# Performance work log

Measured on AMD Instinct MI355X. Metric: run time of the kernel, lower is better.

The kernel has to match this reference:

```python
import math
import jax, jax.numpy as jnp
import numpy as np

B, S, D, H = 2, 2048, 1024, 16
DK = D // H


def setup_inputs() -> dict:
    key = jax.random.key(0)
    ks = jax.random.split(key, 12)
    scale = 1.0 / math.sqrt(D)
    inp = {
        "q": jax.random.normal(ks[0], (B, S, D), jnp.float32),
        "k": jax.random.normal(ks[1], (B, S, D), jnp.float32),
        "v": jax.random.normal(ks[2], (B, S, D), jnp.float32),
        # causal mask, broadcast over batch and heads (mask==0 -> -inf)
        "mask": jnp.tril(jnp.ones((S, S), jnp.int32))[None, None, :, :],
        "Wq": jax.random.normal(ks[3], (D, D), jnp.float32) * scale,
        "bq": jnp.zeros((D,), jnp.float32),
        "Wk": jax.random.normal(ks[4], (D, D), jnp.float32) * scale,
        "bk": jnp.zeros((D,), jnp.float32),
        "Wv": jax.random.normal(ks[5], (D, D), jnp.float32) * scale,
        "bv": jnp.zeros((D,), jnp.float32),
        "Wo": jax.random.normal(ks[6], (D, D), jnp.float32) * scale,
        "bo": jnp.zeros((D,), jnp.float32),
    }
    return inp


def reference(q, k, v, mask, Wq, bq, Wk, bk, Wv, bv, Wo, bo):
    def proj(x, W, b):
        # [B,S,D] -> [B,H,S,DK]
        return (x @ W + b).reshape(B, -1, H, DK).transpose(0, 2, 1, 3)

    Q = proj(q, Wq, bq)
    K = proj(k, Wk, bk)
    V = proj(v, Wv, bv)
    scores = jnp.einsum("bhqd,bhkd->bhqk", Q, K) / math.sqrt(DK)  # [B,H,S,S]
    scores = jnp.where(mask == 0, -jnp.inf, scores)
    attn = jax.nn.softmax(scores, axis=-1)  # dropout p=0.0 -> identity
    ctx = jnp.einsum("bhqk,bhkd->bhqd", attn, V)
    ctx = ctx.transpose(0, 2, 1, 3).reshape(B, -1, D)  # [B,S,D]
    return ctx @ Wo + bo
```

## Files before the change

### kernel.cpp

```cpp
#include <hip/hip_runtime.h>
#include <stdint.h>

#define BB 2
#define SS 2048
#define DD 1024
#define HH 16
#define DK 64

#define QSCALE 0.1803368801111204f
#define NEGS -1.0e30f

typedef short s16x8 __attribute__((ext_vector_type(8)));
typedef float f32x4 __attribute__((ext_vector_type(4)));
typedef unsigned short u16x4 __attribute__((ext_vector_type(4)));
typedef unsigned int u32x4 __attribute__((ext_vector_type(4)));

static __device__ __forceinline__ unsigned short f2bf(float f) {
  unsigned int u = __builtin_bit_cast(unsigned int, f);
  u = (u + 0x7fffu + ((u >> 16) & 1u)) >> 16;
  return (unsigned short)u;
}

static __device__ __forceinline__ float bf2f(unsigned short s) {
  unsigned int u = ((unsigned int)s) << 16;
  return __builtin_bit_cast(float, u);
}

static __device__ __forceinline__ unsigned int cvtpk(float lo, float hi) {
  unsigned int r;
  asm("v_cvt_pk_bf16_f32 %0, %1, %2" : "=v"(r) : "v"(lo), "v"(hi));
  return r;
}

static __device__ __forceinline__ f32x4 mfma16(s16x8 a, s16x8 b, f32x4 c) {
  return __builtin_amdgcn_mfma_f32_16x16x32_bf16(a, b, c, 0, 0, 0);
}

static __device__ __forceinline__ void gload_lds16(const void* g, void* l) {
  __builtin_amdgcn_global_load_lds(
      (const __attribute__((address_space(1))) unsigned int*)g,
      (__attribute__((address_space(3))) unsigned int*)l, 16, 0, 0);
}

__global__ __launch_bounds__(256) void cvt3_kernel(const float* __restrict__ q,
                                                   const float* __restrict__ k,
                                                   const float* __restrict__ v,
                                                   unsigned short* __restrict__ qb,
                                                   unsigned short* __restrict__ kb,
                                                   unsigned short* __restrict__ vb) {
  int sel = blockIdx.y;
  const float* in = (sel == 0) ? q : ((sel == 1) ? k : v);
  unsigned short* out = (sel == 0) ? qb : ((sel == 1) ? kb : vb);
  int i = blockIdx.x * 256 + threadIdx.x;
  f32x4 vv = ((const f32x4*)in)[i];
  u16x4 o;
  o.x = f2bf(vv.x); o.y = f2bf(vv.y); o.z = f2bf(vv.z); o.w = f2bf(vv.w);
  ((u16x4*)out)[i] = o;
}

__global__ __launch_bounds__(256) void transpose_w4_kernel(const float* __restrict__ Wq,
                                                           const float* __restrict__ Wk,
                                                           const float* __restrict__ Wv,
                                                           const float* __restrict__ Wo,
                                                           unsigned short* __restrict__ WTbase) {
  __shared__ float t[32][33];
  int z = blockIdx.z;
  const float* W = (z == 0) ? Wq : ((z == 1) ? Wk : ((z == 2) ? Wv : Wo));
  float scale = (z == 0) ? QSCALE : 1.0f;
  unsigned short* WT = WTbase + (size_t)z * DD * DD;
  int n0 = blockIdx.x * 32, k0 = blockIdx.y * 32;
  int tx = threadIdx.x, ty = threadIdx.y;
  for (int i = 0; i < 4; ++i)
    t[ty + 8 * i][tx] = W[(size_t)(k0 + ty + 8 * i) * DD + n0 + tx];
  __syncthreads();
  for (int i = 0; i < 4; ++i)
    WT[(size_t)(n0 + ty + 8 * i) * DD + k0 + tx] = f2bf(t[tx][ty + 8 * i] * scale);
}

__global__ __launch_bounds__(256) void gemm_qkv_kernel(
    const unsigned short* __restrict__ qb, const unsigned short* __restrict__ kb,
    const unsigned short* __restrict__ vb, const unsigned short* __restrict__ WTbase,
    const float* __restrict__ bq, const float* __restrict__ bk,
    const float* __restrict__ bv, unsigned short* __restrict__ Qh,
    unsigned short* __restrict__ Kh, unsigned short* __restrict__ VhT) {
  const int K = DD;
  __shared__ __align__(16) unsigned short Alds[128 * 32];
  __shared__ __align__(16) unsigned short Blds[128 * 32];
  int tid = threadIdx.x;
  int lane = tid & 63, wave = tid >> 6;
  int g = lane >> 4, r16 = lane & 15;

  int bid = blockIdx.x;
  int logical = (bid & 7) * 96 + (bid >> 3);
  int y = logical >> 3, xn = logical & 7;
  int seg = y >> 5;
  int m0 = (y & 31) * 128, n0 = xn * 128;
  int wm = (wave >> 1) * 64, wn = (wave & 1) * 64;

  const unsigned short* A = (seg == 0) ? qb : ((seg == 1) ? kb : vb);
  const unsigned short* BT = WTbase + (size_t)seg * DD * DD;
  const float* bias = (seg == 0) ? bq : ((seg == 1) ? bk : bv);
  float bsc = (seg == 0) ? QSCALE : 1.0f;

  f32x4 acc[4][4] = {};

  int c0 = tid, c1 = tid + 256;
  int arow0 = c0 >> 2, arow1 = c1 >> 2;
  int as0 = (c0 & 3) ^ ((arow0 >> 1) & 3);
  int as1 = (c1 & 3) ^ ((arow1 >> 1) & 3);

  for (int k0 = 0; k0 < K; k0 += 32) {
    __syncthreads();
    gload_lds16((const char*)(A + (size_t)(m0 + arow0) * K + k0) + as0 * 16,
                (char*)Alds + wave * 1024);
    gload_lds16((const char*)(A + (size_t)(m0 + arow1) * K + k0) + as1 * 16,
                (char*)Alds + wave * 1024 + 4096);
    gload_lds16((const char*)(BT + (size_t)(n0 + arow0) * K + k0) + as0 * 16,
                (char*)Blds + wave * 1024);
    gload_lds16((const char*)(BT + (size_t)(n0 + arow1) * K + k0) + as1 * 16,
                (char*)Blds + wave * 1024 + 4096);
    __syncthreads();

    s16x8 af[4], bfr[4];
#pragma unroll
    for (int mt = 0; mt < 4; ++mt) {
      int row = wm + mt * 16 + r16;
      int ch = g ^ ((row >> 1) & 3);
      af[mt] = *(const s16x8*)((const char*)Alds + row * 64 + ch * 16);
    }
#pragma unroll
    for (int nt = 0; nt < 4; ++nt) {
      int row = wn + nt * 16 + r16;
      int ch = g ^ ((row >> 1) & 3);
      bfr[nt] = *(const s16x8*)((const char*)Blds + row * 64 + ch * 16);
    }
#pragma unroll
    for (int mt = 0; mt < 4; ++mt)
#pragma unroll
      for (int nt = 0; nt < 4; ++nt)
        acc[mt][nt] = mfma16(af[mt], bfr[nt], acc[mt][nt]);
  }

  unsigned short* outh = (seg == 0) ? Qh : Kh;
#pragma unroll
  for (int nt = 0; nt < 4; ++nt) {
    int col = n0 + wn + nt * 16 + r16;
    int h = col >> 6, dk = col & (DK - 1);
    float bvv = bias[col] * bsc;
#pragma unroll
    for (int mt = 0; mt < 4; ++mt) {
      int row0g = m0 + wm + mt * 16 + g * 4;
      int bb = row0g >> 11, s0 = row0g & (SS - 1);
      if (seg == 2) {
        u16x4 o;
#pragma unroll
        for (int rr = 0; rr < 4; ++rr) o[rr] = f2bf(acc[mt][nt][rr] + bvv);
        *(u16x4*)&VhT[((size_t)(bb * HH + h) * DK + dk) * SS + s0] = o;
      } else {
#pragma unroll
        for (int rr = 0; rr < 4; ++rr) {
          outh[(((size_t)bb * HH + h) * SS + s0 + rr) * DK + dk] =
              f2bf(acc[mt][nt][rr] + bvv);
        }
      }
    }
  }
}

__global__ __launch_bounds__(256) void gemm_out_kernel(const unsigned short* __restrict__ A,
                                                       const unsigned short* __restrict__ BT,
                                                       const float* __restrict__ bias,
                                                       float* __restrict__ out) {
  const int K = DD;
  __shared__ __align__(16) unsigned short Alds[128 * 32];
  __shared__ __align__(16) unsigned short Blds[64 * 32];
  int tid = threadIdx.x;
  int lane = tid & 63, wave = tid >> 6;
  int g = lane >> 4, r16 = lane & 15;

  int bid = blockIdx.x;
  int logical = (bid & 7) * 64 + (bid >> 3);
  int m0 = (logical >> 4) * 128, n0 = (logical & 15) * 64;
  int wm = (wave >> 1) * 64, wn = (wave & 1) * 32;

  f32x4 acc[4][2] = {};

  int c0 = tid, c1 = tid + 256;
  int arow0 = c0 >> 2, arow1 = c1 >> 2;
  int as0 = (c0 & 3) ^ ((arow0 >> 1) & 3);
  int as1 = (c1 & 3) ^ ((arow1 >> 1) & 3);

  for (int k0 = 0; k0 < K; k0 += 32) {
    __syncthreads();
    gload_lds16((const char*)(A + (size_t)(m0 + arow0) * K + k0) + as0 * 16,
                (char*)Alds + wave * 1024);
    gload_lds16((const char*)(A + (size_t)(m0 + arow1) * K + k0) + as1 * 16,
                (char*)Alds + wave * 1024 + 4096);
    gload_lds16((const char*)(BT + (size_t)(n0 + arow0) * K + k0) + as0 * 16,
                (char*)Blds + wave * 1024);
    __syncthreads();

    s16x8 af[4], bfr[2];
#pragma unroll
    for (int mt = 0; mt < 4; ++mt) {
      int row = wm + mt * 16 + r16;
      int ch = g ^ ((row >> 1) & 3);
      af[mt] = *(const s16x8*)((const char*)Alds + row * 64 + ch * 16);
    }
#pragma unroll
    for (int nt = 0; nt < 2; ++nt) {
      int row = wn + nt * 16 + r16;
      int ch = g ^ ((row >> 1) & 3);
      bfr[nt] = *(const s16x8*)((const char*)Blds + row * 64 + ch * 16);
    }
#pragma unroll
    for (int mt = 0; mt < 4; ++mt)
#pragma unroll
      for (int nt = 0; nt < 2; ++nt)
        acc[mt][nt] = mfma16(af[mt], bfr[nt], acc[mt][nt]);
  }

#pragma unroll
  for (int nt = 0; nt < 2; ++nt) {
    int col = n0 + wn + nt * 16 + r16;
    float bvv = bias[col];
#pragma unroll
    for (int mt = 0; mt < 4; ++mt) {
#pragma unroll
      for (int rr = 0; rr < 4; ++rr) {
        int rowg = m0 + wm + mt * 16 + g * 4 + rr;
        out[(size_t)rowg * DD + col] = acc[mt][nt][rr] + bvv;
      }
    }
  }
}

__global__ __launch_bounds__(256) void attn_kernel(const unsigned short* __restrict__ Qh,
                                                   const unsigned short* __restrict__ Kh,
                                                   const unsigned short* __restrict__ VhT,
                                                   unsigned short* __restrict__ ctx,
                                                   unsigned short* __restrict__ Opart,
                                                   float2* __restrict__ mlpart) {
  __shared__ __align__(16) unsigned short Klds[2][64 * 64];
  __shared__ __align__(16) unsigned short Vlds[2][64 * 64];

  int tid = threadIdx.x;
  int lane = tid & 63, wave = tid >> 6;
  int g = lane >> 4, r16 = lane & 15;
  int bid = blockIdx.x;
  int x = bid >> 3;
  int pid = x & 7;
  int hf = (x >> 3) & 1;
  int bh = ((x >> 4) << 3) | (bid & 7);

  int tilesA = hf ? 0 : 2 * pid + 2;
  const int NT = 17;
  int q0A = pid * 128, q0B = (15 - pid) * 128;
  int kvoffB = hf ? (15 - 2 * pid) : 0;

  const unsigned short* Qb = Qh + (size_t)bh * SS * DK;
  const char* Kb = (const char*)(Kh + (size_t)bh * SS * DK);
  const char* Vb = (const char*)(VhT + (size_t)bh * DK * SS);

  int a_ = r16 >> 2, b_ = r16 & 3;
  int rbase = 8 * a_ + b_;
  int sk = b_ + 4 * (a_ & 1);

  int c0 = tid, c1 = tid + 256;
  int row0 = c0 >> 3, row1 = c1 >> 3;
  int skst0 = ((row0 & 3) | (((row0 >> 3) & 1) << 2));
  int skst1 = ((row1 & 3) | (((row1 >> 3) & 1) << 2));
  int kc0 = (c0 & 7) ^ skst0, kc1 = (c1 & 7) ^ skst1;
  int vc0 = (c0 & 7) ^ (row0 & 7), vc1 = (c1 & 7) ^ (row1 & 7);

#define KV_OF(t) ((hf ? (kvoffB + (t)) : (((t) < tilesA) ? (t) : ((t) - tilesA))) * 64)
#define STAGE_KV(buf, kv0)                                                   \
  do {                                                                       \
    gload_lds16(Kb + ((size_t)((kv0) + row0) * 128) + kc0 * 16,              \
                (char*)Klds[buf] + wave * 1024);                             \
    gload_lds16(Kb + ((size_t)((kv0) + row1) * 128) + kc1 * 16,              \
                (char*)Klds[buf] + wave * 1024 + 4096);                      \
    gload_lds16(Vb + ((size_t)row0 * SS + (kv0)) * 2 + vc0 * 16,             \
                (char*)Vlds[buf] + wave * 1024);                             \
    gload_lds16(Vb + ((size_t)row1 * SS + (kv0)) * 2 + vc1 * 16,             \
                (char*)Vlds[buf] + wave * 1024 + 4096);                      \
  } while (0)

  int b = bh >> 4, h = bh & (HH - 1);

  int qw0 = (hf ? q0B : q0A) + wave * 32;
  s16x8 aq[2][2];
#pragma unroll
  for (int mt = 0; mt < 2; ++mt)
#pragma unroll
    for (int kc = 0; kc < 2; ++kc)
      aq[mt][kc] = *(const s16x8*)(Qb + (size_t)(qw0 + mt * 16 + r16) * DK + kc * 32 + g * 8);

  STAGE_KV(0, KV_OF(0));

  f32x4 accd[2][4] = {};
  float mrow[2] = {-INFINITY, -INFINITY};
  float lrow[2] = {0.0f, 0.0f};

  for (int t = 0; t < NT; ++t) {
    if (hf == 0 && t == tilesA) {
#pragma unroll
      for (int mt = 0; mt < 2; ++mt) {
        float inv = 1.0f / lrow[mt];
        int srow = qw0 + mt * 16 + r16;
#pragma unroll
        for (int dsub = 0; dsub < 4; ++dsub) {
          int d0 = dsub * 16 + 4 * g;
          u16x4 o;
#pragma unroll
          for (int rr = 0; rr < 4; ++rr) o[rr] = f2bf(accd[mt][dsub][rr] * inv);
          *(u16x4*)&ctx[(((size_t)b * SS + srow) * HH + h) * DK + d0] = o;
        }
      }
      qw0 = q0B + wave * 32;
#pragma unroll
      for (int mt = 0; mt < 2; ++mt)
#pragma unroll
        for (int kc = 0; kc < 2; ++kc)
          aq[mt][kc] = *(const s16x8*)(Qb + (size_t)(qw0 + mt * 16 + r16) * DK + kc * 32 + g * 8);
#pragma unroll
      for (int mt = 0; mt < 2; ++mt) {
#pragma unroll
        for (int dsub = 0; dsub < 4; ++dsub) accd[mt][dsub] = (f32x4){0.f, 0.f, 0.f, 0.f};
        mrow[mt] = -INFINITY;
        lrow[mt] = 0.0f;
      }
    }

    int kv0 = KV_OF(t);

    __syncthreads();
    if (t + 1 < NT) STAGE_KV((t + 1) & 1, KV_OF(t + 1));

    const char* Kc = (const char*)Klds[t & 1];
    const char* Vc = (const char*)Vlds[t & 1];

    f32x4 sf[2][4] = {};
    __builtin_amdgcn_s_setprio(1);
#pragma unroll
    for (int kc = 0; kc < 2; ++kc) {
      s16x8 bk[4];
#pragma unroll
      for (int nt = 0; nt < 4; ++nt) {
        int row = rbase + 4 * (nt & 1) + 32 * (nt >> 1);
        int ch = (kc * 4 + g) ^ sk;
        bk[nt] = *(const s16x8*)(Kc + row * 128 + ch * 16);
      }
#pragma unroll
      for (int nt = 0; nt < 4; ++nt) {
        sf[0][nt] = mfma16(bk[nt], aq[0][kc], sf[0][nt]);
        sf[1][nt] = mfma16(bk[nt], aq[1][kc], sf[1][nt]);
      }
    }
    __builtin_amdgcn_s_setprio(0);

    s16x8 av[2][4];
#pragma unroll
    for (int c = 0; c < 2; ++c)
#pragma unroll
      for (int dsub = 0; dsub < 4; ++dsub) {
        int row = dsub * 16 + r16;
        int ch = (c * 4 + g) ^ (row & 7);
        av[c][dsub] = *(const s16x8*)(Vc + row * 128 + ch * 16);
      }

    bool domask = (kv0 + 63 > qw0);
    unsigned int pk[2][2][4];
#pragma unroll
    for (int mt = 0; mt < 2; ++mt) {
      if (domask) {
        int thr = qw0 + mt * 16 + r16 - kv0 - 8 * g;
#pragma unroll
        for (int nt = 0; nt < 4; ++nt) {
          int koff = 4 * (nt & 1) + 32 * (nt >> 1);
#pragma unroll
          for (int rr = 0; rr < 4; ++rr)
            if (koff + rr > thr) sf[mt][nt][rr] = NEGS;
        }
      }

      float m0v = fmaxf(fmaxf(sf[mt][0][0], sf[mt][0][1]), fmaxf(sf[mt][0][2], sf[mt][0][3]));
      float m1v = fmaxf(fmaxf(sf[mt][1][0], sf[mt][1][1]), fmaxf(sf[mt][1][2], sf[mt][1][3]));
      float m2v = fmaxf(fmaxf(sf[mt][2][0], sf[mt][2][1]), fmaxf(sf[mt][2][2], sf[mt][2][3]));
      float m3v = fmaxf(fmaxf(sf[mt][3][0], sf[mt][3][1]), fmaxf(sf[mt][3][2], sf[mt][3][3]));
      float tmax = fmaxf(fmaxf(m0v, m1v), fmaxf(m2v, m3v));
      tmax = fmaxf(tmax, __shfl_xor(tmax, 16));
      tmax = fmaxf(tmax, __shfl_xor(tmax, 32));

      if (!__all(tmax <= mrow[mt])) {
        float mn = fmaxf(mrow[mt], tmax);
        float fc = __builtin_amdgcn_exp2f(mrow[mt] - mn);
        lrow[mt] *= fc;
        mrow[mt] = mn;
#pragma unroll
        for (int dsub = 0; dsub < 4; ++dsub)
#pragma unroll
          for (int rr = 0; rr < 4; ++rr) accd[mt][dsub][rr] *= fc;
      }

      float pf[4][4];
#pragma unroll
      for (int nt = 0; nt < 4; ++nt)
#pragma unroll
        for (int rr = 0; rr < 4; ++rr)
          pf[nt][rr] = __builtin_amdgcn_exp2f(sf[mt][nt][rr] - mrow[mt]);
      float s0v = (pf[0][0] + pf[0][1]) + (pf[0][2] + pf[0][3]);
      float s1v = (pf[1][0] + pf[1][1]) + (pf[1][2] + pf[1][3]);
      float s2v = (pf[2][0] + pf[2][1]) + (pf[2][2] + pf[2][3]);
      float s3v = (pf[3][0] + pf[3][1]) + (pf[3][2] + pf[3][3]);
      float su = (s0v + s1v) + (s2v + s3v);
      su += __shfl_xor(su, 16);
      su += __shfl_xor(su, 32);
      lrow[mt] += su;

#pragma unroll
      for (int c = 0; c < 2; ++c) {
        pk[mt][c][0] = cvtpk(pf[2 * c][0], pf[2 * c][1]);
        pk[mt][c][1] = cvtpk(pf[2 * c][2], pf[2 * c][3]);
        pk[mt][c][2] = cvtpk(pf[2 * c + 1][0], pf[2 * c + 1][1]);
        pk[mt][c][3] = cvtpk(pf[2 * c + 1][2], pf[2 * c + 1][3]);
      }
    }

    __builtin_amdgcn_s_setprio(1);
#pragma unroll
    for (int c = 0; c < 2; ++c) {
      s16x8 pb0 = __builtin_bit_cast(s16x8, *(u32x4*)pk[0][c]);
      s16x8 pb1 = __builtin_bit_cast(s16x8, *(u32x4*)pk[1][c]);
#pragma unroll
      for (int dsub = 0; dsub < 4; ++dsub) {
        accd[0][dsub] = mfma16(av[c][dsub], pb0, accd[0][dsub]);
        accd[1][dsub] = mfma16(av[c][dsub], pb1, accd[1][dsub]);
      }
    }
    __builtin_amdgcn_s_setprio(0);
  }

#pragma unroll
  for (int mt = 0; mt < 2; ++mt) {
    size_t prow = ((size_t)bh * 8 + pid) * 128 + wave * 32 + mt * 16 + r16;
    float inv = 1.0f / lrow[mt];
    unsigned short* Op = Opart + ((size_t)hf * 32768 + prow) * 64;
#pragma unroll
    for (int dsub = 0; dsub < 4; ++dsub) {
      int d0 = dsub * 16 + 4 * g;
      u16x4 o;
#pragma unroll
      for (int rr = 0; rr < 4; ++rr) o[rr] = f2bf(accd[mt][dsub][rr] * inv);
      *(u16x4*)&Op[d0] = o;
    }
    if (g == 0) mlpart[(size_t)hf * 32768 + prow] = make_float2(mrow[mt], lrow[mt]);
  }
#undef STAGE_KV
#undef KV_OF
}

__global__ __launch_bounds__(256) void combine_kernel(const unsigned short* __restrict__ Opart,
                                                      const float2* __restrict__ mlpart,
                                                      unsigned short* __restrict__ ctx) {
  int idx = blockIdx.x * 256 + threadIdx.x;
  int row = idx >> 4;
  int d0 = (idx & 15) * 4;
  float2 ml0 = mlpart[row];
  float2 ml1 = mlpart[32768 + row];
  float m = fmaxf(ml0.x, ml1.x);
  float w0 = __builtin_amdgcn_exp2f(ml0.x - m) * ml0.y;
  float w1 = __builtin_amdgcn_exp2f(ml1.x - m) * ml1.y;
  float inv = 1.0f / (w0 + w1);
  w0 *= inv;
  w1 *= inv;
  u16x4 a = *(const u16x4*)(Opart + (size_t)row * 64 + d0);
  u16x4 bb4 = *(const u16x4*)(Opart + ((size_t)32768 + row) * 64 + d0);
  u16x4 o;
#pragma unroll
  for (int j = 0; j < 4; ++j) o[j] = f2bf(bf2f(a[j]) * w0 + bf2f(bb4[j]) * w1);
  int p = row >> 7, rin = row & 127;
  int bh = p >> 3, pid = p & 7;
  int srow = (15 - pid) * 128 + rin;
  int b = bh >> 4, h = bh & (HH - 1);
  *(u16x4*)&ctx[(((size_t)b * SS + srow) * HH + h) * DK + d0] = o;
}

extern "C" void kernel_launch(void* const* d_in, const int* in_sizes, int n_in,
                              void* d_out, int out_size, void* d_ws, size_t ws_size,
                              hipStream_t stream) {
  const float* q = (const float*)d_in[0];
  const float* k = (const float*)d_in[1];
  const float* v = (const float*)d_in[2];
  const float* Wq = (const float*)d_in[4];
  const float* bq = (const float*)d_in[5];
  const float* Wk = (const float*)d_in[6];
  const float* bk = (const float*)d_in[7];
  const float* Wv = (const float*)d_in[8];
  const float* bv = (const float*)d_in[9];
  const float* Wo = (const float*)d_in[10];
  const float* bo = (const float*)d_in[11];

  char* ws = (char*)d_ws;
  const size_t MB = 1ull << 20;
  unsigned short* qb = (unsigned short*)(ws + 0 * MB);
  unsigned short* kb = (unsigned short*)(ws + 8 * MB);
  unsigned short* vb = (unsigned short*)(ws + 16 * MB);
  unsigned short* WTbase = (unsigned short*)(ws + 24 * MB);
  unsigned short* WoT = (unsigned short*)(ws + 30 * MB);
  unsigned short* Qh = (unsigned short*)(ws + 32 * MB);
  unsigned short* Kh = (unsigned short*)(ws + 40 * MB);
  unsigned short* VhT = (unsigned short*)(ws + 48 * MB);
  unsigned short* ctx = (unsigned short*)(ws + 0 * MB);
  unsigned short* Opart = (unsigned short*)(ws + 8 * MB);
  float2* mlpart = (float2*)(ws + 24 * MB);

  const int n4 = BB * SS * DD / 4;

  cvt3_kernel<<<dim3(n4 / 256, 3), 256, 0, stream>>>(q, k, v, qb, kb, vb);

  dim3 tb(32, 8);
  transpose_w4_kernel<<<dim3(32, 32, 4), tb, 0, stream>>>(Wq, Wk, Wv, Wo, WTbase);

  gemm_qkv_kernel<<<768, 256, 0, stream>>>(qb, kb, vb, WTbase,
                                           bq, bk, bv, Qh, Kh, VhT);

  attn_kernel<<<512, 256, 0, stream>>>(Qh, Kh, VhT, ctx, Opart, mlpart);

  combine_kernel<<<2048, 256, 0, stream>>>(Opart, mlpart, ctx);

  gemm_out_kernel<<<512, 256, 0, stream>>>(ctx, WoT, bo, (float*)d_out);
}
```

Baseline: 133.6 us.

## Double-buffer LDS tiles in projection GEMMs and raise priority around MFMAs

Both the QKV projection GEMM and the output projection GEMM now keep two LDS buffers. The next k-tile's global-to-LDS loads are issued before computing on the current tile, and the loop needs one barrier per iteration instead of two. The MFMA block is wrapped in s_setprio so compute waves get scheduling priority. This hides global load latency behind matrix math, at the cost of doubling LDS per block, which may lower occupancy.

```diff
diff --git a/kernel.cpp b/kernel.cpp
--- a/kernel.cpp
+++ b/kernel.cpp
@@ -84,8 +84,8 @@
     const float* __restrict__ bv, unsigned short* __restrict__ Qh,
     unsigned short* __restrict__ Kh, unsigned short* __restrict__ VhT) {
   const int K = DD;
-  __shared__ __align__(16) unsigned short Alds[128 * 32];
-  __shared__ __align__(16) unsigned short Blds[128 * 32];
+  __shared__ __align__(16) unsigned short Alds[2][128 * 32];
+  __shared__ __align__(16) unsigned short Blds[2][128 * 32];
   int tid = threadIdx.x;
   int lane = tid & 63, wave = tid >> 6;
   int g = lane >> 4, r16 = lane & 15;
@@ -109,37 +109,48 @@
   int as0 = (c0 & 3) ^ ((arow0 >> 1) & 3);
   int as1 = (c1 & 3) ^ ((arow1 >> 1) & 3);
 
+#define STAGE_AB(buf, k0)                                                        \
+  do {                                                                           \
+    gload_lds16((const char*)(A + (size_t)(m0 + arow0) * K + (k0)) + as0 * 16,   \
+                (char*)Alds[buf] + wave * 1024);                                 \
+    gload_lds16((const char*)(A + (size_t)(m0 + arow1) * K + (k0)) + as1 * 16,   \
+                (char*)Alds[buf] + wave * 1024 + 4096);                          \
+    gload_lds16((const char*)(BT + (size_t)(n0 + arow0) * K + (k0)) + as0 * 16,  \
+                (char*)Blds[buf] + wave * 1024);                                 \
+    gload_lds16((const char*)(BT + (size_t)(n0 + arow1) * K + (k0)) + as1 * 16,  \
+                (char*)Blds[buf] + wave * 1024 + 4096);                          \
+  } while (0)
+
+  STAGE_AB(0, 0);
+  int cur = 0;
+
   for (int k0 = 0; k0 < K; k0 += 32) {
     __syncthreads();
-    gload_lds16((const char*)(A + (size_t)(m0 + arow0) * K + k0) + as0 * 16,
-                (char*)Alds + wave * 1024);
-    gload_lds16((const char*)(A + (size_t)(m0 + arow1) * K + k0) + as1 * 16,
-                (char*)Alds + wave * 1024 + 4096);
-    gload_lds16((const char*)(BT + (size_t)(n0 + arow0) * K + k0) + as0 * 16,
-                (char*)Blds + wave * 1024);
-    gload_lds16((const char*)(BT + (size_t)(n0 + arow1) * K + k0) + as1 * 16,
-                (char*)Blds + wave * 1024 + 4096);
-    __syncthreads();
+    if (k0 + 32 < K) STAGE_AB(cur ^ 1, k0 + 32);
 
     s16x8 af[4], bfr[4];
 #pragma unroll
     for (int mt = 0; mt < 4; ++mt) {
       int row = wm + mt * 16 + r16;
       int ch = g ^ ((row >> 1) & 3);
-      af[mt] = *(const s16x8*)((const char*)Alds + row * 64 + ch * 16);
+      af[mt] = *(const s16x8*)((const char*)Alds[cur] + row * 64 + ch * 16);
     }
 #pragma unroll
     for (int nt = 0; nt < 4; ++nt) {
       int row = wn + nt * 16 + r16;
       int ch = g ^ ((row >> 1) & 3);
-      bfr[nt] = *(const s16x8*)((const char*)Blds + row * 64 + ch * 16);
-    }
+      bfr[nt] = *(const s16x8*)((const char*)Blds[cur] + row * 64 + ch * 16);
+    }
+    __builtin_amdgcn_s_setprio(1);
 #pragma unroll
     for (int mt = 0; mt < 4; ++mt)
 #pragma unroll
       for (int nt = 0; nt < 4; ++nt)
         acc[mt][nt] = mfma16(af[mt], bfr[nt], acc[mt][nt]);
+    __builtin_amdgcn_s_setprio(0);
+    cur ^= 1;
   }
+#undef STAGE_AB
 
   unsigned short* outh = (seg == 0) ? Qh : Kh;
 #pragma unroll
@@ -172,8 +183,8 @@
                                                        const float* __restrict__ bias,
                                                        float* __restrict__ out) {
   const int K = DD;
-  __shared__ __align__(16) unsigned short Alds[128 * 32];
-  __shared__ __align__(16) unsigned short Blds[64 * 32];
+  __shared__ __align__(16) unsigned short Alds[2][128 * 32];
+  __shared__ __align__(16) unsigned short Blds[2][64 * 32];
   int tid = threadIdx.x;
   int lane = tid & 63, wave = tid >> 6;
   int g = lane >> 4, r16 = lane & 15;
@@ -190,35 +201,46 @@
   int as0 = (c0 & 3) ^ ((arow0 >> 1) & 3);
   int as1 = (c1 & 3) ^ ((arow1 >> 1) & 3);
 
+#define STAGE_AB(buf, k0)                                                        \
+  do {                                                                           \
+    gload_lds16((const char*)(A + (size_t)(m0 + arow0) * K + (k0)) + as0 * 16,   \
+                (char*)Alds[buf] + wave * 1024);                                 \
+    gload_lds16((const char*)(A + (size_t)(m0 + arow1) * K + (k0)) + as1 * 16,   \
+                (char*)Alds[buf] + wave * 1024 + 4096);                          \
+    gload_lds16((const char*)(BT + (size_t)(n0 + arow0) * K + (k0)) + as0 * 16,  \
+                (char*)Blds[buf] + wave * 1024);                                 \
+  } while (0)
+
+  STAGE_AB(0, 0);
+  int cur = 0;
+
   for (int k0 = 0; k0 < K; k0 += 32) {
     __syncthreads();
-    gload_lds16((const char*)(A + (size_t)(m0 + arow0) * K + k0) + as0 * 16,
-                (char*)Alds + wave * 1024);
-    gload_lds16((const char*)(A + (size_t)(m0 + arow1) * K + k0) + as1 * 16,
-                (char*)Alds + wave * 1024 + 4096);
-    gload_lds16((const char*)(BT + (size_t)(n0 + arow0) * K + k0) + as0 * 16,
-                (char*)Blds + wave * 1024);
-    __syncthreads();
+    if (k0 + 32 < K) STAGE_AB(cur ^ 1, k0 + 32);
 
     s16x8 af[4], bfr[2];
 #pragma unroll
     for (int mt = 0; mt < 4; ++mt) {
       int row = wm + mt * 16 + r16;
       int ch = g ^ ((row >> 1) & 3);
-      af[mt] = *(const s16x8*)((const char*)Alds + row * 64 + ch * 16);
+      af[mt] = *(const s16x8*)((const char*)Alds[cur] + row * 64 + ch * 16);
     }
 #pragma unroll
     for (int nt = 0; nt < 2; ++nt) {
       int row = wn + nt * 16 + r16;
       int ch = g ^ ((row >> 1) & 3);
-      bfr[nt] = *(const s16x8*)((const char*)Blds + row * 64 + ch * 16);
-    }
+      bfr[nt] = *(const s16x8*)((const char*)Blds[cur] + row * 64 + ch * 16);
+    }
+    __builtin_amdgcn_s_setprio(1);
 #pragma unroll
     for (int mt = 0; mt < 4; ++mt)
 #pragma unroll
       for (int nt = 0; nt < 2; ++nt)
         acc[mt][nt] = mfma16(af[mt], bfr[nt], acc[mt][nt]);
+    __builtin_amdgcn_s_setprio(0);
+    cur ^= 1;
   }
+#undef STAGE_AB
 
 #pragma unroll
   for (int nt = 0; nt < 2; ++nt) {
```

Result: faster. 119.7 us (-10.4%).
